# Kernel optimization log

Measured on AMD Instinct MI355X. Metric: run time of the kernel, lower is better.

## Reference

```python
import jax, jax.numpy as jnp
import numpy as np

N = 100000   # nodes
E = 1600000  # edges
NC = 10000   # candidates
G = 1000     # graphs
ND = 32      # node_emb_dim
ED = 8       # edge_emb_dim
L = 4        # num_layers


def setup_inputs() -> dict:
    key = jax.random.key(0)
    ks = jax.random.split(key, 12)
    s = 0.1
    return {
        "x": jax.random.normal(ks[0], (N, 2), dtype=jnp.float32),
        "edge_attr": jax.random.normal(ks[1], (E, 1), dtype=jnp.float32),
        "Wn_in": jax.random.normal(ks[2], (2, ND)) * s,
        "bn_in": jnp.zeros((ND,)),
        "We_in": jax.random.normal(ks[3], (1, ED)) * s,
        "be_in": jnp.zeros((ED,)),
        "We_l": jax.random.normal(ks[4], (L, 2 * ND + ED, ED)) * s,
        "be_l": jnp.zeros((L, ED)),
        "Wn_l": jax.random.normal(ks[5], (L, ND + ED, ND)) * s,
        "bn_l": jnp.zeros((L, ND)),
        "Wout": jax.random.normal(ks[6], (ND, 1)) * s,
        "bout": jnp.zeros((1,)),
        "edge_index": jax.random.randint(ks[7], (2, E), 0, N),
        "batch": jnp.sort(jax.random.randint(ks[8], (N,), 0, G)),
        "candidate_idxs": jax.random.randint(ks[9], (NC,), 0, N),
    }


def reference(x, edge_attr, Wn_in, bn_in, We_in, be_in, We_l, be_l, Wn_l, bn_l,
              Wout, bout, edge_index, batch, candidate_idxs):
    h = x @ Wn_in + bn_in            # [N, ND]
    e = edge_attr @ We_in + be_in    # [E, ED]
    src, dst = edge_index[0], edge_index[1]
    for l in range(L):
        # edge update: MLP on [x_src, x_dst, edge_attr]
        m = jnp.concatenate([h[src], h[dst], e], axis=-1)        # [E, 2*ND+ED]
        new_e = jax.nn.relu(m @ We_l[l] + be_l[l])               # [E, ED]
        # aggregate (aggr='add') messages at destination nodes
        agg = jax.ops.segment_sum(new_e, dst, num_segments=N)    # [N, ED]
        new_h = jax.nn.relu(jnp.concatenate([h, agg], axis=-1) @ Wn_l[l] + bn_l[l])
        h = h + new_h   # residual
        e = e + new_e   # residual
    logits = (h[candidate_idxs] @ Wout + bout)[:, 0]             # [NC]
    seg = batch[candidate_idxs]                                  # [NC] graph ids
    # scatter_log_softmax over per-graph candidate groups
    mx = jax.ops.segment_max(logits, seg, num_segments=G)
    shifted = logits - mx[seg]
    lse = jnp.log(jax.ops.segment_sum(jnp.exp(shifted), seg, num_segments=G))
    return shifted - lse[seg]
```

## Files before the change

kernel.cpp:

```cpp
#include <hip/hip_runtime.h>

#define ND 32
#define ED 8
#define NL 4
#define NG 1000
#define NBC_MAX 512
#define CHUNK 8192
#define CHUNK_H 4096
#define NBLK 64

typedef unsigned short u16;

__device__ __forceinline__ int xcd_swizzle(int b, int nb) {
  int per = nb >> 3;
  return (b < (per << 3)) ? ((b & 7) * per + (b >> 3)) : b;
}


__device__ __forceinline__ u16 f2bf(float f) {
  unsigned u = __float_as_uint(f);
  u += 0x7fffu + ((u >> 16) & 1u);
  return (u16)(u >> 16);
}
__device__ __forceinline__ unsigned pack2(float a, float b) {
  return (unsigned)f2bf(a) | ((unsigned)f2bf(b) << 16);
}
__device__ __forceinline__ void cvt8(uint4 p, float* o) {
  o[0] = __uint_as_float(p.x << 16); o[1] = __uint_as_float(p.x & 0xffff0000u);
  o[2] = __uint_as_float(p.y << 16); o[3] = __uint_as_float(p.y & 0xffff0000u);
  o[4] = __uint_as_float(p.z << 16); o[5] = __uint_as_float(p.z & 0xffff0000u);
  o[6] = __uint_as_float(p.w << 16); o[7] = __uint_as_float(p.w & 0xffff0000u);
}
__device__ __forceinline__ uint4 pack8(const float* v) {
  uint4 o;
  o.x = pack2(v[0], v[1]); o.y = pack2(v[2], v[3]);
  o.z = pack2(v[4], v[5]); o.w = pack2(v[6], v[7]);
  return o;
}


__global__ void k_init_h(const float* __restrict__ x,
                         const float* __restrict__ W,
                         const float* __restrict__ b,
                         const float* __restrict__ We,
                         const float* __restrict__ be,
                         u16* __restrict__ h,
                         u16* __restrict__ zs, u16* __restrict__ zd,
                         int N) {
  int n = xcd_swizzle(blockIdx.x, gridDim.x) * blockDim.x + threadIdx.x;
  if (n >= N) return;
  float x0 = x[2 * n], x1 = x[2 * n + 1];
  float v[ND];
#pragma unroll
  for (int d = 0; d < ND; ++d) v[d] = fmaf(x0, W[d], fmaf(x1, W[ND + d], b[d]));
#pragma unroll
  for (int d = 0; d < ND; ++d) v[d] = __uint_as_float((unsigned)f2bf(v[d]) << 16);
  uint4* h4 = reinterpret_cast<uint4*>(h + (size_t)n * ND);
#pragma unroll
  for (int q = 0; q < 4; ++q) h4[q] = pack8(&v[q * 8]);
  float zsv[ED], zdv[ED];
#pragma unroll
  for (int j = 0; j < ED; ++j) { zsv[j] = 0.0f; zdv[j] = be[j]; }
#pragma unroll
  for (int k = 0; k < ND; ++k)
#pragma unroll
    for (int j = 0; j < ED; ++j) {
      zsv[j] = fmaf(v[k], We[k * ED + j], zsv[j]);
      zdv[j] = fmaf(v[k], We[(ND + k) * ED + j], zdv[j]);
    }
  *reinterpret_cast<uint4*>(zs + (size_t)n * ED) = pack8(zsv);
  *reinterpret_cast<uint4*>(zd + (size_t)n * ED) = pack8(zdv);
}


__global__ void k_chist(const int* __restrict__ dst, int* __restrict__ bcnt,
                        int E, int nbc) {
  __shared__ int lcnt[NBC_MAX];
  for (int b = threadIdx.x; b < nbc; b += blockDim.x) lcnt[b] = 0;
  __syncthreads();
  int e0 = blockIdx.x * CHUNK_H;
  int e1 = min(e0 + CHUNK_H, E);
  for (int i = e0 + threadIdx.x; i < e1; i += blockDim.x)
    atomicAdd(&lcnt[dst[i] >> 8], 1);
  __syncthreads();
  for (int b = threadIdx.x; b < nbc; b += blockDim.x)
    if (lcnt[b]) atomicAdd(&bcnt[b], lcnt[b]);
}

__global__ void k_cscan(const int* __restrict__ bcnt, int* __restrict__ bbase,
                        int nbc) {
  __shared__ int s[NBC_MAX];
  int tid = threadIdx.x;
  if (nbc <= NBC_MAX) {
    int v = (tid < nbc) ? bcnt[tid] : 0;
    s[tid] = v;
    __syncthreads();
    for (int st = 1; st < NBC_MAX; st <<= 1) {
      int t = (tid >= st) ? s[tid - st] : 0;
      __syncthreads();
      s[tid] += t;
      __syncthreads();
    }
    if (tid < nbc) bbase[tid] = s[tid] - v;
    if (tid == nbc - 1) bbase[nbc] = s[tid];
  } else if (tid == 0) {
    int run = 0;
    for (int i = 0; i < nbc; ++i) { bbase[i] = run; run += bcnt[i]; }
    bbase[nbc] = run;
  }
}

__global__ void k_binA(const int* __restrict__ src, const int* __restrict__ dst,
                       const float* __restrict__ ea,
                       const int* __restrict__ bbase, int* __restrict__ cursor_c,
                       uint2* __restrict__ binned, int E, int nbc) {
  __shared__ int lcnt[NBC_MAX];
  __shared__ int lbase[NBC_MAX];
  for (int b = threadIdx.x; b < nbc; b += blockDim.x) lcnt[b] = 0;
  __syncthreads();
  int e0 = blockIdx.x * CHUNK;
  int e1 = min(e0 + CHUNK, E);
  for (int i = e0 + threadIdx.x; i < e1; i += blockDim.x)
    atomicAdd(&lcnt[dst[i] >> 8], 1);
  __syncthreads();
  for (int b = threadIdx.x; b < nbc; b += blockDim.x) {
    int c = lcnt[b];
    lbase[b] = c ? (bbase[b] + atomicAdd(&cursor_c[b], c)) : 0;
  }
  __syncthreads();
  for (int i = e0 + threadIdx.x; i < e1; i += blockDim.x) {
    int d = dst[i];
    int pos = atomicAdd(&lbase[d >> 8], 1);
    binned[pos] = make_uint2((unsigned)src[i] | ((unsigned)(d & 255) << 24),
                             __float_as_uint(ea[i]));
  }
}

__global__ void k_binB(const uint2* __restrict__ binned,
                       const int* __restrict__ bbase,
                       uint2* __restrict__ sedge, u16* __restrict__ e,
                       int* __restrict__ noffs,
                       const float* __restrict__ We,
                       const float* __restrict__ be,
                       int N) {
  __shared__ int hist[256];
  __shared__ int scn[256];
  int b = blockIdx.x;
  int base = bbase[b], end = bbase[b + 1];
  int node0 = b << 8;
  int nn = min(256, N - node0);
  hist[threadIdx.x] = 0;
  __syncthreads();
  for (int p = base + threadIdx.x; p < end; p += blockDim.x)
    atomicAdd(&hist[binned[p].x >> 24], 1);
  __syncthreads();
  int v = hist[threadIdx.x];
  scn[threadIdx.x] = v;
  __syncthreads();
  for (int st = 1; st < 256; st <<= 1) {
    int t = (threadIdx.x >= (unsigned)st) ? scn[threadIdx.x - st] : 0;
    __syncthreads();
    scn[threadIdx.x] += t;
    __syncthreads();
  }
  int excl = base + scn[threadIdx.x] - v;
  if ((int)threadIdx.x < nn) noffs[node0 + threadIdx.x] = excl;
  if (threadIdx.x == 0) noffs[min(node0 + 256, N)] = end;
  hist[threadIdx.x] = excl;
  __syncthreads();
  for (int p = base + threadIdx.x; p < end; p += blockDim.x) {
    uint2 rec = binned[p];
    int dl = (int)(rec.x >> 24);
    int pos = atomicAdd(&hist[dl], 1);
    sedge[pos] = make_uint2(rec.x & 0xffffffu, (unsigned)(node0 + dl));
    float a = __uint_as_float(rec.y);
    float e0[ED];
#pragma unroll
    for (int j = 0; j < ED; ++j) e0[j] = fmaf(a, We[j], be[j]);
    *reinterpret_cast<uint4*>(e + (size_t)pos * ED) = pack8(e0);
  }
}


__global__ void k_edge(const u16* __restrict__ zs,
                       const u16* __restrict__ zd,
                       u16* __restrict__ e,
                       u16* __restrict__ ne,
                       const uint2* __restrict__ sedge,
                       const float* __restrict__ W3,
                       int E) {
  int i = xcd_swizzle(blockIdx.x, gridDim.x) * blockDim.x + threadIdx.x;
  if (i >= E) return;
  uint2 sd = sedge[i];
  float zsv[ED], zdv[ED], ein[ED], acc[ED];
  cvt8(*reinterpret_cast<const uint4*>(zs + (size_t)sd.x * ED), zsv);
  cvt8(*reinterpret_cast<const uint4*>(zd + (size_t)sd.y * ED), zdv);
  cvt8(*reinterpret_cast<const uint4*>(e + (size_t)i * ED), ein);
#pragma unroll
  for (int j = 0; j < ED; ++j) acc[j] = zsv[j] + zdv[j];
#pragma unroll
  for (int k = 0; k < ED; ++k)
#pragma unroll
    for (int j = 0; j < ED; ++j)
      acc[j] = fmaf(ein[k], W3[k * ED + j], acc[j]);
#pragma unroll
  for (int j = 0; j < ED; ++j) acc[j] = fmaxf(acc[j], 0.0f);
  *reinterpret_cast<uint4*>(ne + (size_t)i * ED) = pack8(acc);
  float eo[ED];
#pragma unroll
  for (int j = 0; j < ED; ++j) eo[j] = ein[j] + acc[j];
  *reinterpret_cast<uint4*>(e + (size_t)i * ED) = pack8(eo);
}

__global__ void k_node(u16* __restrict__ h,
                       const u16* __restrict__ ne,
                       const int* __restrict__ noffs,
                       const float* __restrict__ W,
                       const float* __restrict__ b,
                       const float* __restrict__ Wen,
                       const float* __restrict__ ben,
                       u16* __restrict__ zs, u16* __restrict__ zd,
                       int N) {
  int n = xcd_swizzle(blockIdx.x, gridDim.x) * blockDim.x + threadIdx.x;
  if (n >= N) return;
  int o0 = noffs[n], o1 = noffs[n + 1];
  float av[ED];
#pragma unroll
  for (int j = 0; j < ED; ++j) av[j] = 0.0f;
  int p = o0;
  for (; p + 3 < o1; p += 4) {
    uint4 r0 = *reinterpret_cast<const uint4*>(ne + (size_t)(p + 0) * ED);
    uint4 r1 = *reinterpret_cast<const uint4*>(ne + (size_t)(p + 1) * ED);
    uint4 r2 = *reinterpret_cast<const uint4*>(ne + (size_t)(p + 2) * ED);
    uint4 r3 = *reinterpret_cast<const uint4*>(ne + (size_t)(p + 3) * ED);
    float t0[ED], t1[ED], t2[ED], t3[ED];
    cvt8(r0, t0); cvt8(r1, t1); cvt8(r2, t2); cvt8(r3, t3);
#pragma unroll
    for (int j = 0; j < ED; ++j)
      av[j] += (t0[j] + t1[j]) + (t2[j] + t3[j]);
  }
  for (; p < o1; ++p) {
    float t[ED];
    cvt8(*reinterpret_cast<const uint4*>(ne + (size_t)p * ED), t);
#pragma unroll
    for (int j = 0; j < ED; ++j) av[j] += t[j];
  }
  float acc[ND];
#pragma unroll
  for (int j = 0; j < ND; ++j) acc[j] = b[j];
  uint4* h4 = reinterpret_cast<uint4*>(h + (size_t)n * ND);
  float hv[ND];
#pragma unroll
  for (int q = 0; q < 4; ++q) cvt8(h4[q], &hv[q * 8]);
#pragma unroll
  for (int k = 0; k < ND; ++k)
#pragma unroll
    for (int j = 0; j < ND; ++j) acc[j] = fmaf(hv[k], W[k * ND + j], acc[j]);
#pragma unroll
  for (int k = 0; k < ED; ++k)
#pragma unroll
    for (int j = 0; j < ND; ++j) acc[j] = fmaf(av[k], W[(ND + k) * ND + j], acc[j]);
  float hn[ND];
#pragma unroll
  for (int k = 0; k < ND; ++k) {
    float o = hv[k] + fmaxf(acc[k], 0.0f);
    hn[k] = __uint_as_float((unsigned)f2bf(o) << 16);
  }
#pragma unroll
  for (int q = 0; q < 4; ++q) h4[q] = pack8(&hn[q * 8]);
  float zsv[ED], zdv[ED];
#pragma unroll
  for (int j = 0; j < ED; ++j) { zsv[j] = 0.0f; zdv[j] = ben[j]; }
#pragma unroll
  for (int k = 0; k < ND; ++k)
#pragma unroll
    for (int j = 0; j < ED; ++j) {
      zsv[j] = fmaf(hn[k], Wen[k * ED + j], zsv[j]);
      zdv[j] = fmaf(hn[k], Wen[(ND + k) * ED + j], zdv[j]);
    }
  *reinterpret_cast<uint4*>(zs + (size_t)n * ED) = pack8(zsv);
  *reinterpret_cast<uint4*>(zd + (size_t)n * ED) = pack8(zdv);
}


__device__ __forceinline__ unsigned int enc_f32(float f) {
  unsigned int bits = __float_as_uint(f);
  return (bits & 0x80000000u) ? ~bits : (bits | 0x80000000u);
}
__device__ __forceinline__ float dec_f32(unsigned int u) {
  unsigned int bits = (u & 0x80000000u) ? (u ^ 0x80000000u) : ~u;
  return __uint_as_float(bits);
}

__global__ void k_cand(const u16* __restrict__ h,
                       const u16* __restrict__ e,
                       const u16* __restrict__ zs,
                       const u16* __restrict__ zd,
                       const uint2* __restrict__ sedge,
                       const int* __restrict__ noffs,
                       const int* __restrict__ cand,
                       const int* __restrict__ batch,
                       const float* __restrict__ W3,
                       const float* __restrict__ Wn,
                       const float* __restrict__ bn,
                       const float* __restrict__ Wout,
                       const float* __restrict__ bout,
                       float* __restrict__ logits,
                       int* __restrict__ seg,
                       unsigned int* __restrict__ mxu,
                       int NC) {
  int c = blockIdx.x * blockDim.x + threadIdx.x;
  if (c >= NC) return;
  int n = cand[c];
  int o0 = noffs[n], o1 = noffs[n + 1];
  float zdv[ED];
  cvt8(*reinterpret_cast<const uint4*>(zd + (size_t)n * ED), zdv);
  float av[ED];
#pragma unroll
  for (int j = 0; j < ED; ++j) av[j] = 0.0f;
  for (int p = o0; p < o1; ++p) {
    unsigned s = sedge[p].x;
    float zsv[ED], ein[ED], acc[ED];
    cvt8(*reinterpret_cast<const uint4*>(zs + (size_t)s * ED), zsv);
    cvt8(*reinterpret_cast<const uint4*>(e + (size_t)p * ED), ein);
#pragma unroll
    for (int j = 0; j < ED; ++j) acc[j] = zsv[j] + zdv[j];
#pragma unroll
    for (int k = 0; k < ED; ++k)
#pragma unroll
      for (int j = 0; j < ED; ++j)
        acc[j] = fmaf(ein[k], W3[k * ED + j], acc[j]);
#pragma unroll
    for (int j = 0; j < ED; ++j) av[j] += fmaxf(acc[j], 0.0f);
  }
  float acc[ND];
#pragma unroll
  for (int j = 0; j < ND; ++j) acc[j] = bn[j];
  const uint4* h4 = reinterpret_cast<const uint4*>(h + (size_t)n * ND);
  float hv[ND];
#pragma unroll
  for (int q = 0; q < 4; ++q) cvt8(h4[q], &hv[q * 8]);
#pragma unroll
  for (int k = 0; k < ND; ++k)
#pragma unroll
    for (int j = 0; j < ND; ++j) acc[j] = fmaf(hv[k], Wn[k * ND + j], acc[j]);
#pragma unroll
  for (int k = 0; k < ED; ++k)
#pragma unroll
    for (int j = 0; j < ND; ++j) acc[j] = fmaf(av[k], Wn[(ND + k) * ND + j], acc[j]);
  float lg = bout[0];
#pragma unroll
  for (int k = 0; k < ND; ++k)
    lg = fmaf(hv[k] + fmaxf(acc[k], 0.0f), Wout[k], lg);
  logits[c] = lg;
  int g = batch[n];
  seg[c] = g;
  atomicMax(&mxu[g], enc_f32(lg));
}

__global__ void k_expsum(float* __restrict__ logits,
                         const int* __restrict__ seg,
                         const unsigned int* __restrict__ mxu,
                         float* __restrict__ sum,
                         int NC) {
  int c = blockIdx.x * blockDim.x + threadIdx.x;
  if (c >= NC) return;
  int g = seg[c];
  float sh = logits[c] - dec_f32(mxu[g]);
  logits[c] = sh;
  atomicAdd(&sum[g], expf(sh));
}

__global__ void k_final(const float* __restrict__ shifted,
                        const int* __restrict__ seg,
                        const float* __restrict__ sum,
                        float* __restrict__ out, int NC) {
  int c = blockIdx.x * blockDim.x + threadIdx.x;
  if (c >= NC) return;
  out[c] = shifted[c] - logf(sum[seg[c]]);
}


extern "C" void kernel_launch(void* const* d_in, const int* in_sizes, int n_in,
                              void* d_out, int out_size, void* d_ws, size_t ws_size,
                              hipStream_t stream) {
  const float* x       = (const float*)d_in[0];
  const float* ea      = (const float*)d_in[1];
  const float* Wn_in   = (const float*)d_in[2];
  const float* bn_in   = (const float*)d_in[3];
  const float* We_in   = (const float*)d_in[4];
  const float* be_in   = (const float*)d_in[5];
  const float* We_l    = (const float*)d_in[6];
  const float* be_l    = (const float*)d_in[7];
  const float* Wn_l    = (const float*)d_in[8];
  const float* bn_l    = (const float*)d_in[9];
  const float* Wout    = (const float*)d_in[10];
  const float* bout    = (const float*)d_in[11];
  const int* edge_index= (const int*)d_in[12];
  const int* batch     = (const int*)d_in[13];
  const int* cand      = (const int*)d_in[14];

  const int N  = in_sizes[13];
  const int E  = in_sizes[1];
  const int NC = in_sizes[14];
  const int nbc = (N + 255) >> 8;

  char* ws = (char*)d_ws;
  uint2* binned = (uint2*)ws; ws += (size_t)E * sizeof(uint2);
  uint2* sedge  = (uint2*)ws; ws += (size_t)E * sizeof(uint2);
  u16*   h      = (u16*)ws;   ws += (size_t)N * ND * sizeof(u16);
  u16*   e      = (u16*)ws;   ws += (size_t)E * ED * sizeof(u16);
  u16*   ne     = (u16*)ws;   ws += (size_t)E * ED * sizeof(u16);
  u16*   zs     = (u16*)ws;   ws += (size_t)N * ED * sizeof(u16);
  u16*   zd     = (u16*)ws;   ws += (size_t)N * ED * sizeof(u16);
  int*   noffs  = (int*)ws;   ws += ((size_t)N + 4) * sizeof(int);
  int*   bcnt   = (int*)ws;   ws += (size_t)NBC_MAX * sizeof(int);
  int*   cursor = (int*)ws;   ws += (size_t)NBC_MAX * sizeof(int);
  int*   bbase  = (int*)ws;   ws += ((size_t)NBC_MAX + 4) * sizeof(int);
  float* logits = (float*)ws; ws += (size_t)NC * sizeof(float);
  int*   seg    = (int*)ws;   ws += (size_t)NC * sizeof(int);
  unsigned int* mxu = (unsigned int*)ws; ws += (size_t)NG * sizeof(unsigned int);
  float* sum    = (float*)ws; ws += (size_t)NG * sizeof(float);

  const int* srcp = edge_index;
  const int* dstp = edge_index + E;
  const int blk = 256;
  const size_t WE_STRIDE = (size_t)(2 * ND + ED) * ED;

  hipMemsetAsync(bcnt, 0, 2 * (size_t)NBC_MAX * sizeof(int), stream);
  k_chist<<<(E + CHUNK_H - 1) / CHUNK_H, 1024, 0, stream>>>(dstp, bcnt, E, nbc);
  k_cscan<<<1, NBC_MAX, 0, stream>>>(bcnt, bbase, nbc);
  k_binA<<<(E + CHUNK - 1) / CHUNK, 1024, 0, stream>>>(srcp, dstp, ea, bbase,
                                                       cursor, binned, E, nbc);
  k_binB<<<nbc, 256, 0, stream>>>(binned, bbase, sedge, e, noffs, We_in, be_in, N);

  k_init_h<<<(N + NBLK - 1) / NBLK, NBLK, 0, stream>>>(x, Wn_in, bn_in, We_l,
                                                       be_l, h, zs, zd, N);

  const int egrid = (E + blk - 1) / blk;
  const int ngrid = (N + NBLK - 1) / NBLK;
  for (int l = 0; l < NL - 1; ++l) {
    const float* W3 = We_l + l * WE_STRIDE + (size_t)2 * ND * ED;
    const float* Wn = Wn_l + (size_t)l * (ND + ED) * ND;
    const float* bn = bn_l + (size_t)l * ND;
    k_edge<<<egrid, blk, 0, stream>>>(zs, zd, e, ne, sedge, W3, E);
    k_node<<<ngrid, NBLK, 0, stream>>>(
        h, ne, noffs, Wn, bn, We_l + (l + 1) * WE_STRIDE,
        be_l + (size_t)(l + 1) * ED, zs, zd, N);
  }

  hipMemsetAsync(mxu, 0, NG * (sizeof(unsigned int) + sizeof(float)), stream);
  {
    const int l = NL - 1;
    const float* W3 = We_l + l * WE_STRIDE + (size_t)2 * ND * ED;
    const float* Wn = Wn_l + (size_t)l * (ND + ED) * ND;
    const float* bn = bn_l + (size_t)l * ND;
    k_cand<<<(NC + NBLK - 1) / NBLK, NBLK, 0, stream>>>(
        h, e, zs, zd, sedge, noffs, cand, batch, W3, Wn, bn, Wout, bout,
        logits, seg, mxu, NC);
  }
  k_expsum<<<(NC + blk - 1) / blk, blk, 0, stream>>>(logits, seg, mxu, sum, NC);
  k_final<<<(NC + blk - 1) / blk, blk, 0, stream>>>(logits, seg, sum,
                                                    (float*)d_out, NC);
}
```

Baseline: 342.2 us.

## Fuse edge update into per-node layer kernel and drop ne buffer

Merges the per-edge update kernel and the per-node aggregation kernel into one per-destination-node kernel. It computes each incoming edge's message on the fly, accumulates it into the aggregate, and writes back the residual edge state. This removes the ne intermediate buffer, the separate edge launch, and the per-edge destination index. Layer 0 builds the initial edge embedding from the raw attribute instead of materialising it in binning. z buffers are double-buffered so one node's writes don't race with other nodes' reads. The trade-off is that edge work is now serialised per node thread, giving load imbalance with variable degree and fewer parallel threads doing the edge math.

Result: slower. 365.8 us (+6.9%).

```diff
diff --git a/kernel.cpp b/kernel.cpp
--- a/kernel.cpp
+++ b/kernel.cpp
@@ -138,10 +138,8 @@
 
 __global__ void k_binB(const uint2* __restrict__ binned,
                        const int* __restrict__ bbase,
-                       uint2* __restrict__ sedge, u16* __restrict__ e,
+                       int* __restrict__ ssrc, float* __restrict__ ea_s,
                        int* __restrict__ noffs,
-                       const float* __restrict__ We,
-                       const float* __restrict__ be,
                        int N) {
   __shared__ int hist[256];
   __shared__ int scn[256];
@@ -172,82 +170,68 @@
     uint2 rec = binned[p];
     int dl = (int)(rec.x >> 24);
     int pos = atomicAdd(&hist[dl], 1);
-    sedge[pos] = make_uint2(rec.x & 0xffffffu, (unsigned)(node0 + dl));
-    float a = __uint_as_float(rec.y);
-    float e0[ED];
-#pragma unroll
-    for (int j = 0; j < ED; ++j) e0[j] = fmaf(a, We[j], be[j]);
-    *reinterpret_cast<uint4*>(e + (size_t)pos * ED) = pack8(e0);
-  }
-}
-
-
-__global__ void k_edge(const u16* __restrict__ zs,
-                       const u16* __restrict__ zd,
-                       u16* __restrict__ e,
-                       u16* __restrict__ ne,
-                       const uint2* __restrict__ sedge,
-                       const float* __restrict__ W3,
-                       int E) {
-  int i = xcd_swizzle(blockIdx.x, gridDim.x) * blockDim.x + threadIdx.x;
-  if (i >= E) return;
-  uint2 sd = sedge[i];
-  float zsv[ED], zdv[ED], ein[ED], acc[ED];
-  cvt8(*reinterpret_cast<const uint4*>(zs + (size_t)sd.x * ED), zsv);
-  cvt8(*reinterpret_cast<const uint4*>(zd + (size_t)sd.y * ED), zdv);
-  cvt8(*reinterpret_cast<const uint4*>(e + (size_t)i * ED), ein);
-#pragma unroll
-  for (int j = 0; j < ED; ++j) acc[j] = zsv[j] + zdv[j];
-#pragma unroll
-  for (int k = 0; k < ED; ++k)
-#pragma unroll
-    for (int j = 0; j < ED; ++j)
-      acc[j] = fmaf(ein[k], W3[k * ED + j], acc[j]);
-#pragma unroll
-  for (int j = 0; j < ED; ++j) acc[j] = fmaxf(acc[j], 0.0f);
-  *reinterpret_cast<uint4*>(ne + (size_t)i * ED) = pack8(acc);
-  float eo[ED];
-#pragma unroll
-  for (int j = 0; j < ED; ++j) eo[j] = ein[j] + acc[j];
-  *reinterpret_cast<uint4*>(e + (size_t)i * ED) = pack8(eo);
-}
-
-__global__ void k_node(u16* __restrict__ h,
-                       const u16* __restrict__ ne,
-                       const int* __restrict__ noffs,
-                       const float* __restrict__ W,
-                       const float* __restrict__ b,
-                       const float* __restrict__ Wen,
-                       const float* __restrict__ ben,
-                       u16* __restrict__ zs, u16* __restrict__ zd,
-                       int N) {
+    ssrc[pos] = (int)(rec.x & 0xffffffu);
+    ea_s[pos] = __uint_as_float(rec.y);
+  }
+}
+
+template <int L0>
+__global__ void k_layer(u16* __restrict__ h,
+                        u16* __restrict__ e,
+                        const float* __restrict__ ea_s,
+                        const int* __restrict__ ssrc,
+                        const int* __restrict__ noffs,
+                        const u16* __restrict__ zs,
+                        const u16* __restrict__ zd,
+                        const float* __restrict__ Wei,
+                        const float* __restrict__ bei,
+                        const float* __restrict__ W3,
+                        const float* __restrict__ Wn,
+                        const float* __restrict__ bn,
+                        const float* __restrict__ Wen,
+                        const float* __restrict__ ben,
+                        u16* __restrict__ zs_n, u16* __restrict__ zd_n,
+                        int N) {
   int n = xcd_swizzle(blockIdx.x, gridDim.x) * blockDim.x + threadIdx.x;
   if (n >= N) return;
   int o0 = noffs[n], o1 = noffs[n + 1];
+  float zdv[ED];
+  cvt8(*reinterpret_cast<const uint4*>(zd + (size_t)n * ED), zdv);
   float av[ED];
 #pragma unroll
   for (int j = 0; j < ED; ++j) av[j] = 0.0f;
-  int p = o0;
-  for (; p + 3 < o1; p += 4) {
-    uint4 r0 = *reinterpret_cast<const uint4*>(ne + (size_t)(p + 0) * ED);
-    uint4 r1 = *reinterpret_cast<const uint4*>(ne + (size_t)(p + 1) * ED);
-    uint4 r2 = *reinterpret_cast<const uint4*>(ne + (size_t)(p + 2) * ED);
-    uint4 r3 = *reinterpret_cast<const uint4*>(ne + (size_t)(p + 3) * ED);
-    float t0[ED], t1[ED], t2[ED], t3[ED];
-    cvt8(r0, t0); cvt8(r1, t1); cvt8(r2, t2); cvt8(r3, t3);
-#pragma unroll
-    for (int j = 0; j < ED; ++j)
-      av[j] += (t0[j] + t1[j]) + (t2[j] + t3[j]);
-  }
-  for (; p < o1; ++p) {
-    float t[ED];
-    cvt8(*reinterpret_cast<const uint4*>(ne + (size_t)p * ED), t);
-#pragma unroll
-    for (int j = 0; j < ED; ++j) av[j] += t[j];
+  for (int p = o0; p < o1; ++p) {
+    int s = ssrc[p];
+    float zsv[ED];
+    cvt8(*reinterpret_cast<const uint4*>(zs + (size_t)s * ED), zsv);
+    float ein[ED];
+    if (L0) {
+      float a = ea_s[p];
+#pragma unroll
+      for (int j = 0; j < ED; ++j) ein[j] = fmaf(a, Wei[j], bei[j]);
+    } else {
+      cvt8(*reinterpret_cast<const uint4*>(e + (size_t)p * ED), ein);
+    }
+    float acc[ED];
+#pragma unroll
+    for (int j = 0; j < ED; ++j) acc[j] = zsv[j] + zdv[j];
+#pragma unroll
+    for (int k = 0; k < ED; ++k)
+#pragma unroll
+      for (int j = 0; j < ED; ++j)
+        acc[j] = fmaf(ein[k], W3[k * ED + j], acc[j]);
+    float eo[ED];
+#pragma unroll
+    for (int j = 0; j < ED; ++j) {
+      float r = fmaxf(acc[j], 0.0f);
+      av[j] += r;
+      eo[j] = ein[j] + r;
+    }
+    *reinterpret_cast<uint4*>(e + (size_t)p * ED) = pack8(eo);
   }
   float acc[ND];
 #pragma unroll
-  for (int j = 0; j < ND; ++j) acc[j] = b[j];
+  for (int j = 0; j < ND; ++j) acc[j] = bn[j];
   uint4* h4 = reinterpret_cast<uint4*>(h + (size_t)n * ND);
   float hv[ND];
 #pragma unroll
@@ -255,11 +239,11 @@
 #pragma unroll
   for (int k = 0; k < ND; ++k)
 #pragma unroll
-    for (int j = 0; j < ND; ++j) acc[j] = fmaf(hv[k], W[k * ND + j], acc[j]);
+    for (int j = 0; j < ND; ++j) acc[j] = fmaf(hv[k], Wn[k * ND + j], acc[j]);
 #pragma unroll
   for (int k = 0; k < ED; ++k)
 #pragma unroll
-    for (int j = 0; j < ND; ++j) acc[j] = fmaf(av[k], W[(ND + k) * ND + j], acc[j]);
+    for (int j = 0; j < ND; ++j) acc[j] = fmaf(av[k], Wn[(ND + k) * ND + j], acc[j]);
   float hn[ND];
 #pragma unroll
   for (int k = 0; k < ND; ++k) {
@@ -268,18 +252,18 @@
   }
 #pragma unroll
   for (int q = 0; q < 4; ++q) h4[q] = pack8(&hn[q * 8]);
-  float zsv[ED], zdv[ED];
-#pragma unroll
-  for (int j = 0; j < ED; ++j) { zsv[j] = 0.0f; zdv[j] = ben[j]; }
+  float zsv[ED], zdv2[ED];
+#pragma unroll
+  for (int j = 0; j < ED; ++j) { zsv[j] = 0.0f; zdv2[j] = ben[j]; }
 #pragma unroll
   for (int k = 0; k < ND; ++k)
 #pragma unroll
     for (int j = 0; j < ED; ++j) {
       zsv[j] = fmaf(hn[k], Wen[k * ED + j], zsv[j]);
-      zdv[j] = fmaf(hn[k], Wen[(ND + k) * ED + j], zdv[j]);
-    }
-  *reinterpret_cast<uint4*>(zs + (size_t)n * ED) = pack8(zsv);
-  *reinterpret_cast<uint4*>(zd + (size_t)n * ED) = pack8(zdv);
+      zdv2[j] = fmaf(hn[k], Wen[(ND + k) * ED + j], zdv2[j]);
+    }
+  *reinterpret_cast<uint4*>(zs_n + (size_t)n * ED) = pack8(zsv);
+  *reinterpret_cast<uint4*>(zd_n + (size_t)n * ED) = pack8(zdv2);
 }
 
 
@@ -296,7 +280,7 @@
                        const u16* __restrict__ e,
                        const u16* __restrict__ zs,
                        const u16* __restrict__ zd,
-                       const uint2* __restrict__ sedge,
+                       const int* __restrict__ ssrc,
                        const int* __restrict__ noffs,
                        const int* __restrict__ cand,
                        const int* __restrict__ batch,
@@ -319,7 +303,7 @@
 #pragma unroll
   for (int j = 0; j < ED; ++j) av[j] = 0.0f;
   for (int p = o0; p < o1; ++p) {
-    unsigned s = sedge[p].x;
+    int s = ssrc[p];
     float zsv[ED], ein[ED], acc[ED];
     cvt8(*reinterpret_cast<const uint4*>(zs + (size_t)s * ED), zsv);
     cvt8(*reinterpret_cast<const uint4*>(e + (size_t)p * ED), ein);
@@ -407,12 +391,14 @@
 
   char* ws = (char*)d_ws;
   uint2* binned = (uint2*)ws; ws += (size_t)E * sizeof(uint2);
-  uint2* sedge  = (uint2*)ws; ws += (size_t)E * sizeof(uint2);
+  int*   ssrc   = (int*)ws;   ws += (size_t)E * sizeof(int);
+  float* ea_s   = (float*)ws; ws += (size_t)E * sizeof(float);
   u16*   h      = (u16*)ws;   ws += (size_t)N * ND * sizeof(u16);
   u16*   e      = (u16*)ws;   ws += (size_t)E * ED * sizeof(u16);
-  u16*   ne     = (u16*)ws;   ws += (size_t)E * ED * sizeof(u16);
-  u16*   zs     = (u16*)ws;   ws += (size_t)N * ED * sizeof(u16);
-  u16*   zd     = (u16*)ws;   ws += (size_t)N * ED * sizeof(u16);
+  u16*   zs0    = (u16*)ws;   ws += (size_t)N * ED * sizeof(u16);
+  u16*   zd0    = (u16*)ws;   ws += (size_t)N * ED * sizeof(u16);
+  u16*   zs1    = (u16*)ws;   ws += (size_t)N * ED * sizeof(u16);
+  u16*   zd1    = (u16*)ws;   ws += (size_t)N * ED * sizeof(u16);
   int*   noffs  = (int*)ws;   ws += ((size_t)N + 4) * sizeof(int);
   int*   bcnt   = (int*)ws;   ws += (size_t)NBC_MAX * sizeof(int);
   int*   cursor = (int*)ws;   ws += (size_t)NBC_MAX * sizeof(int);
@@ -432,21 +418,32 @@
   k_cscan<<<1, NBC_MAX, 0, stream>>>(bcnt, bbase, nbc);
   k_binA<<<(E + CHUNK - 1) / CHUNK, 1024, 0, stream>>>(srcp, dstp, ea, bbase,
                                                        cursor, binned, E, nbc);
-  k_binB<<<nbc, 256, 0, stream>>>(binned, bbase, sedge, e, noffs, We_in, be_in, N);
+  k_binB<<<nbc, 256, 0, stream>>>(binned, bbase, ssrc, ea_s, noffs, N);
 
   k_init_h<<<(N + NBLK - 1) / NBLK, NBLK, 0, stream>>>(x, Wn_in, bn_in, We_l,
-                                                       be_l, h, zs, zd, N);
-
-  const int egrid = (E + blk - 1) / blk;
+                                                       be_l, h, zs0, zd0, N);
+
   const int ngrid = (N + NBLK - 1) / NBLK;
+  u16* zsc = zs0; u16* zdc = zd0;
+  u16* zsn = zs1; u16* zdn = zd1;
   for (int l = 0; l < NL - 1; ++l) {
     const float* W3 = We_l + l * WE_STRIDE + (size_t)2 * ND * ED;
     const float* Wn = Wn_l + (size_t)l * (ND + ED) * ND;
     const float* bn = bn_l + (size_t)l * ND;
-    k_edge<<<egrid, blk, 0, stream>>>(zs, zd, e, ne, sedge, W3, E);
-    k_node<<<ngrid, NBLK, 0, stream>>>(
-        h, ne, noffs, Wn, bn, We_l + (l + 1) * WE_STRIDE,
-        be_l + (size_t)(l + 1) * ED, zs, zd, N);
+    const float* Wen = We_l + (l + 1) * WE_STRIDE;
+    const float* ben = be_l + (size_t)(l + 1) * ED;
+    if (l == 0) {
+      k_layer<1><<<ngrid, NBLK, 0, stream>>>(
+          h, e, ea_s, ssrc, noffs, zsc, zdc, We_in, be_in, W3, Wn, bn,
+          Wen, ben, zsn, zdn, N);
+    } else {
+      k_layer<0><<<ngrid, NBLK, 0, stream>>>(
+          h, e, ea_s, ssrc, noffs, zsc, zdc, We_in, be_in, W3, Wn, bn,
+          Wen, ben, zsn, zdn, N);
+    }
+    u16* t;
+    t = zsc; zsc = zsn; zsn = t;
+    t = zdc; zdc = zdn; zdn = t;
   }
 
   hipMemsetAsync(mxu, 0, NG * (sizeof(unsigned int) + sizeof(float)), stream);
@@ -456,7 +453,7 @@
     const float* Wn = Wn_l + (size_t)l * (ND + ED) * ND;
     const float* bn = bn_l + (size_t)l * ND;
     k_cand<<<(NC + NBLK - 1) / NBLK, NBLK, 0, stream>>>(
-        h, e, zs, zd, sedge, noffs, cand, batch, W3, Wn, bn, Wout, bout,
+        h, e, zsc, zdc, ssrc, noffs, cand, batch, W3, Wn, bn, Wout, bout,
         logits, seg, mxu, NC);
   }
   k_expsum<<<(NC + blk - 1) / blk, blk, 0, stream>>>(logits, seg, mxu, sum, NC);
```
